# Performance work log

Hardware: AMD Instinct MI355X
Metric: run time of the kernel (lower is better)

The kernel has to match this reference:

```python
import jax, jax.numpy as jnp
import numpy as np

NUM_HEADS = 16
NUM_KV_HEADS = 8
HEAD_DIM = 128
ROPE_THETA = 10000.0
SOFTCAP = 50.0


def rotate_half(x):
    x1, x2 = jnp.split(x, 2, axis=-1)
    return jnp.concatenate((-x2, x1), axis=-1)


def rope_cos_sin(seq_len):
    inv_freq = 1.0 / (ROPE_THETA ** (jnp.arange(0, HEAD_DIM, 2, dtype=jnp.float32) / HEAD_DIM))
    t = jnp.arange(seq_len, dtype=jnp.float32)
    freqs = t[:, None] * inv_freq[None, :]          # [S, D/2]
    emb = jnp.concatenate((freqs, freqs), axis=-1)  # [S, D]
    return jnp.cos(emb), jnp.sin(emb)


def setup_inputs() -> dict:
    key = jax.random.key(0)
    k1, k2, k3, k4, k5 = jax.random.split(key, 5)
    B, S, H = 2, 2048, 2048
    sc = 1.0 / np.sqrt(H)
    return {
        "hidden_states": jax.random.normal(k1, (B, S, H), dtype=jnp.float32),
        "Wq": jax.random.normal(k2, (H, NUM_HEADS * HEAD_DIM), dtype=jnp.float32) * sc,
        "Wk": jax.random.normal(k3, (H, NUM_KV_HEADS * HEAD_DIM), dtype=jnp.float32) * sc,
        "Wv": jax.random.normal(k4, (H, NUM_KV_HEADS * HEAD_DIM), dtype=jnp.float32) * sc,
        "Wo": jax.random.normal(k5, (NUM_HEADS * HEAD_DIM, H), dtype=jnp.float32) * sc,
    }


def reference(hidden_states, Wq, Wk, Wv, Wo):
    B, S, _ = hidden_states.shape
    groups = NUM_HEADS // NUM_KV_HEADS

    # projections -> [B, heads, S, D]
    q = (hidden_states @ Wq).reshape(B, S, NUM_HEADS, HEAD_DIM).transpose(0, 2, 1, 3)
    k = (hidden_states @ Wk).reshape(B, S, NUM_KV_HEADS, HEAD_DIM).transpose(0, 2, 1, 3)
    v = (hidden_states @ Wv).reshape(B, S, NUM_KV_HEADS, HEAD_DIM).transpose(0, 2, 1, 3)

    cos, sin = rope_cos_sin(S)  # [S, D], broadcast over (B, heads)
    q = q * cos + rotate_half(q) * sin
    k = k * cos + rotate_half(k) * sin

    # GQA: expand KV heads (repeat_interleave along head dim)
    k = jnp.repeat(k, groups, axis=1)
    v = jnp.repeat(v, groups, axis=1)

    scores = jnp.einsum('bhsd,bhtd->bhst', q, k) / np.sqrt(HEAD_DIM)
    scores = jnp.tanh(scores / SOFTCAP) * SOFTCAP  # Gemma logit softcapping
    weights = jax.nn.softmax(scores.astype(jnp.float32), axis=-1).astype(q.dtype)

    out = jnp.einsum('bhst,bhtd->bhsd', weights, v)
    out = out.transpose(0, 2, 1, 3).reshape(B, S, NUM_HEADS * HEAD_DIM)
    return out @ Wo
```

## Files before the change

kernel.cpp:

```cpp
#include <hip/hip_runtime.h>
#include <math.h>

typedef __bf16 bf16;
typedef __bf16 bf16x8 __attribute__((ext_vector_type(8)));
typedef __bf16 bf16x4 __attribute__((ext_vector_type(4)));
typedef float f32x2 __attribute__((ext_vector_type(2)));
typedef float f32x4 __attribute__((ext_vector_type(4)));
typedef float f32x16 __attribute__((ext_vector_type(16)));
typedef unsigned int uint;
typedef uint u32x4 __attribute__((ext_vector_type(4)));
typedef uint u32x2 __attribute__((ext_vector_type(2)));
typedef __bf16 bf16x8_a __attribute__((ext_vector_type(8), __may_alias__));
typedef uint u32x2_a __attribute__((ext_vector_type(2), __may_alias__));
typedef __bf16 bf16_a __attribute__((__may_alias__));

constexpr int BATCH = 2;
constexpr int SEQ   = 2048;
constexpr int HID   = 2048;
constexpr int NHEAD = 16;
constexpr int NKV   = 8;
constexpr int HD    = 128;
constexpr int MROWS = BATCH * SEQ;

#define DEVINL __device__ __forceinline__

#define BAR()                                 \
  do {                                        \
    asm volatile("" ::: "memory");            \
    __builtin_amdgcn_s_barrier();             \
    asm volatile("" ::: "memory");            \
  } while (0)

#define WAITV(N) asm volatile("s_waitcnt vmcnt(" #N ")" ::: "memory")

DEVINL void async16(void* l, const void* g) {
  __builtin_amdgcn_global_load_lds((const __attribute__((address_space(1))) void*)g,
                                   (__attribute__((address_space(3))) void*)l, 16, 0, 0);
}

DEVINL f32x4 mfma16(bf16x8 a, bf16x8 b, f32x4 c) {
  return __builtin_amdgcn_mfma_f32_16x16x32_bf16(a, b, c, 0, 0, 0);
}
DEVINL f32x16 mfma32(bf16x8 a, bf16x8 b, f32x16 c) {
  return __builtin_amdgcn_mfma_f32_32x32x16_bf16(a, b, c, 0, 0, 0);
}

DEVINL f32x4 fzero4() { f32x4 z; z[0] = 0.f; z[1] = 0.f; z[2] = 0.f; z[3] = 0.f; return z; }

DEVINL float ex2(float x) {
#if __has_builtin(__builtin_amdgcn_exp2f)
  return __builtin_amdgcn_exp2f(x);
#else
  return __expf(x * 0.6931471805599453f);
#endif
}

DEVINL uint pkbf16(float lo, float hi) {
  unsigned short l = __builtin_bit_cast(unsigned short, (bf16)lo);
  unsigned short h = __builtin_bit_cast(unsigned short, (bf16)hi);
  return (uint)l | ((uint)h << 16);
}

__global__ __launch_bounds__(256) void cast_f32_bf16(const float* __restrict__ x,
                                                     bf16* __restrict__ y, int n) {
  int i = (blockIdx.x * 256 + threadIdx.x) * 4;
  if (i + 3 < n) {
    float4 v = *(const float4*)(x + i);
    bf16x4 o;
    o[0] = (bf16)v.x; o[1] = (bf16)v.y; o[2] = (bf16)v.z; o[3] = (bf16)v.w;
    *(bf16x4*)(y + i) = o;
  }
}

__global__ __launch_bounds__(256) void wtrans4(const float* __restrict__ Wq,
                                               const float* __restrict__ Wk,
                                               const float* __restrict__ Wv,
                                               const float* __restrict__ Wo,
                                               bf16* __restrict__ WqT, bf16* __restrict__ WkT,
                                               bf16* __restrict__ WvT, bf16* __restrict__ WoT) {
  __shared__ bf16 t[64][65];
  const float* W; bf16* WT; int N;
  switch (blockIdx.z) {
    case 0: W = Wq; WT = WqT; N = 2048; break;
    case 1: W = Wk; WT = WkT; N = 1024; break;
    case 2: W = Wv; WT = WvT; N = 1024; break;
    default: W = Wo; WT = WoT; N = 2048; break;
  }
  int n0 = blockIdx.x * 64, k0 = blockIdx.y * 64;
  if (n0 >= N) return;
  for (int i = threadIdx.x; i < 4096; i += 256) {
    int r = i >> 6, c = i & 63;
    t[r][c] = (bf16)W[(size_t)(k0 + r) * N + n0 + c];
  }
  __syncthreads();
  for (int i = threadIdx.x; i < 4096; i += 256) {
    int r = i >> 6, c = i & 63;
    WT[(size_t)(n0 + r) * 2048 + k0 + c] = t[c][r];
  }
}

__global__ __launch_bounds__(256) void vtrans(const bf16* __restrict__ V, bf16* __restrict__ VT) {
  __shared__ bf16 t[64][65];
  int s0 = blockIdx.x * 64, d0 = blockIdx.y * 64;
  int bh = blockIdx.z, b = bh >> 3, kvh = bh & 7;
  for (int i = threadIdx.x; i < 4096; i += 256) {
    int r = i >> 6, c = i & 63;
    t[r][c] = V[(size_t)(b * SEQ + s0 + r) * (NKV * HD) + kvh * HD + d0 + c];
  }
  __syncthreads();
  for (int i = threadIdx.x; i < 4096; i += 256) {
    int r = i >> 6, c = i & 63;
    VT[((size_t)bh * HD + d0 + r) * SEQ + s0 + c] = t[c][r];
  }
}

__global__ void rope_tab(float* __restrict__ ct, float* __restrict__ st) {
  int s = blockIdx.x, d = threadIdx.x;
  float freq = powf(10000.0f, -(float)d * (1.0f / 64.0f));
  float a = (float)s * freq;
  ct[s * 64 + d] = cosf(a);
  st[s * 64 + d] = sinf(a);
}

template <int EPI>
__global__ __launch_bounds__(512, 2) void gemm8p(const bf16* __restrict__ A,
                                                 const bf16* __restrict__ BT,
                                                 void* __restrict__ C0, void* __restrict__ C1,
                                                 void* __restrict__ C2, int M, int N, int K,
                                                 const float* __restrict__ ct,
                                                 const float* __restrict__ st) {
  __shared__ alignas(16) char ldsA[65536];
  __shared__ alignas(16) char ldsB[65536];
  const int tid = threadIdx.x, lane = tid & 63, w = tid >> 6;
  const int l15 = lane & 15, l4 = lane >> 4;
  const int wm = w >> 2, wn = w & 3;
  const int gx = gridDim.x;
  const int nwg = gx * gridDim.y;
  int id = blockIdx.y * gx + blockIdx.x;
  id = (id & 7) * (nwg >> 3) + (id >> 3);
  const int row0 = (id / gx) * 256;
  const int col0 = (id % gx) * 256;

  f32x4 acc[8][4];
#pragma unroll
  for (int mt = 0; mt < 8; mt++)
#pragma unroll
    for (int nt = 0; nt < 4; nt++) acc[mt][nt] = fzero4();

  const int rG0 = tid >> 3, sG0 = ((tid & 7) ^ (rG0 & 7)) * 8;
  const int ci1 = 512 + tid;
  const int rG1 = ci1 >> 3, sG1 = ((ci1 & 7) ^ (rG1 & 7)) * 8;
  const int dst0 = tid * 16, dst1 = (512 + tid) * 16;

  const bf16* Asrc = A + (size_t)row0 * K;
  const bf16* Bsrc = BT + (size_t)col0 * K;
  const int nk = K >> 6;

#define STG_A(half, kt, buf)                                         \
  {                                                                  \
    char* d = ldsA + (buf) * 32768 + (half) * 16384;                 \
    const bf16* s = Asrc + (size_t)((half) * 128) * K + (kt) * 64;   \
    async16(d + dst0, s + (size_t)rG0 * K + sG0);                    \
    async16(d + dst1, s + (size_t)rG1 * K + sG1);                    \
  }
#define STG_B(half, kt, buf)                                         \
  {                                                                  \
    char* d = ldsB + (buf) * 32768 + (half) * 16384;                 \
    const bf16* s = Bsrc + (size_t)((half) * 128) * K + (kt) * 64;   \
    async16(d + dst0, s + (size_t)rG0 * K + sG0);                    \
    async16(d + dst1, s + (size_t)rG1 * K + sG1);                    \
  }

  STG_A(0, 0, 0) STG_A(1, 0, 0) STG_B(0, 0, 0) STG_B(1, 0, 0)
  STG_B(0, 1, 1) STG_B(1, 1, 1) STG_A(0, 1, 1) STG_A(1, 1, 1)
  WAITV(8);
  BAR();

  bf16x8 af[8];
  bf16x8 bfr[2][4];

  for (int t = 0; t < nk; ++t) {
    const int buf = t & 1;
    const char* bA = ldsA + buf * 32768 + wm * 16384;
    const char* bB = ldsB + buf * 32768;
    const bool s2 = (t + 2) < nk;

#pragma unroll
    for (int mtp = 0; mtp < 4; mtp++)
#pragma unroll
      for (int kc = 0; kc < 2; kc++) {
        int r = mtp * 16 + l15;
        int off = ((r << 7) + ((kc * 4 + l4) << 4)) ^ ((r & 7) << 4);
        af[mtp * 2 + kc] = *(const bf16x8_a*)(bA + off);
      }
#pragma unroll
    for (int ntp = 0; ntp < 2; ntp++)
#pragma unroll
      for (int kc = 0; kc < 2; kc++) {
        int c = wn * 16 + ntp * 64 + l15;
        int off = ((c << 7) + ((kc * 4 + l4) << 4)) ^ ((c & 7) << 4);
        bfr[0][ntp * 2 + kc] = *(const bf16x8_a*)(bB + off);
      }
    BAR();
    __builtin_amdgcn_s_setprio(1);
#pragma unroll
    for (int mtp = 0; mtp < 4; mtp++)
#pragma unroll
      for (int ntp = 0; ntp < 2; ntp++)
#pragma unroll
        for (int kc = 0; kc < 2; kc++)
          acc[mtp][ntp] = mfma16(af[mtp * 2 + kc], bfr[0][ntp * 2 + kc], acc[mtp][ntp]);
    __builtin_amdgcn_s_setprio(0);
    BAR();

#pragma unroll
    for (int ntp = 0; ntp < 2; ntp++)
#pragma unroll
      for (int kc = 0; kc < 2; kc++) {
        int c = wn * 16 + ntp * 64 + l15;
        int off = 16384 + (((c << 7) + ((kc * 4 + l4) << 4)) ^ ((c & 7) << 4));
        bfr[1][ntp * 2 + kc] = *(const bf16x8_a*)(bB + off);
      }
    if (s2) STG_B(0, t + 2, buf)
    BAR();
    __builtin_amdgcn_s_setprio(1);
#pragma unroll
    for (int mtp = 0; mtp < 4; mtp++)
#pragma unroll
      for (int ntp = 0; ntp < 2; ntp++)
#pragma unroll
        for (int kc = 0; kc < 2; kc++)
          acc[mtp][ntp + 2] = mfma16(af[mtp * 2 + kc], bfr[1][ntp * 2 + kc], acc[mtp][ntp + 2]);
    __builtin_amdgcn_s_setprio(0);
    BAR();

#pragma unroll
    for (int mtp = 0; mtp < 4; mtp++)
#pragma unroll
      for (int kc = 0; kc < 2; kc++) {
        int r = 64 + mtp * 16 + l15;
        int off = ((r << 7) + ((kc * 4 + l4) << 4)) ^ ((r & 7) << 4);
        af[mtp * 2 + kc] = *(const bf16x8_a*)(bA + off);
      }
    if (s2) STG_B(1, t + 2, buf)
    BAR();
    __builtin_amdgcn_s_setprio(1);
#pragma unroll
    for (int mtp = 0; mtp < 4; mtp++)
#pragma unroll
      for (int ntp = 0; ntp < 2; ntp++)
#pragma unroll
        for (int kc = 0; kc < 2; kc++)
          acc[mtp + 4][ntp + 2] = mfma16(af[mtp * 2 + kc], bfr[1][ntp * 2 + kc], acc[mtp + 4][ntp + 2]);
    __builtin_amdgcn_s_setprio(0);
    BAR();

    if (s2) { STG_A(0, t + 2, buf) STG_A(1, t + 2, buf) }
    BAR();
    __builtin_amdgcn_s_setprio(1);
#pragma unroll
    for (int mtp = 0; mtp < 4; mtp++)
#pragma unroll
      for (int ntp = 0; ntp < 2; ntp++)
#pragma unroll
        for (int kc = 0; kc < 2; kc++)
          acc[mtp + 4][ntp] = mfma16(af[mtp * 2 + kc], bfr[0][ntp * 2 + kc], acc[mtp + 4][ntp]);
    __builtin_amdgcn_s_setprio(0);
    if (s2) { WAITV(8); } else { WAITV(0); }
    BAR();
  }
#undef STG_A
#undef STG_B

#pragma unroll
  for (int mt = 0; mt < 8; mt++)
#pragma unroll
    for (int nt = 0; nt < 4; nt++)
#pragma unroll
      for (int rg = 0; rg < 4; rg++) {
        int row = row0 + wm * 128 + mt * 16 + l4 * 4 + rg;
        int cl = col0 + wn * 16 + nt * 64 + l15;
        float v = acc[mt][nt][rg];
        if (EPI == 2) {
          ((float*)C0)[(size_t)row * N + cl] = v;
        } else {
          if (cl < 3072) {
            int s = row & (SEQ - 1);
            float cc = ct[s * 64 + wn * 16 + l15];
            float ss = st[s * 64 + wn * 16 + l15];
            float pv = acc[mt][nt ^ 1][rg];
            v = (nt & 1) ? fmaf(v, cc, pv * ss) : fmaf(v, cc, -pv * ss);
          }
          if (cl < 2048)
            ((bf16*)C0)[(size_t)row * 2048 + cl] = (bf16)v;
          else if (cl < 3072)
            ((bf16*)C1)[(size_t)row * 1024 + (cl - 2048)] = (bf16)v;
          else
            ((bf16*)C2)[(size_t)row * 1024 + (cl - 3072)] = (bf16)v;
        }
      }
}

__global__ __launch_bounds__(512, 2) void gemm2p(const bf16* __restrict__ A,
                                                 const bf16* __restrict__ BT,
                                                 float* __restrict__ C, int M, int N, int K) {
  __shared__ alignas(16) char ldsA[65536];
  __shared__ alignas(16) char ldsB[32768];
  const int tid = threadIdx.x, lane = tid & 63, w = tid >> 6;
  const int l15 = lane & 15, l4 = lane >> 4;
  const int wm = w >> 1, wn = w & 1;
  const int gx = gridDim.x;
  const int nwg = gx * gridDim.y;
  int id = blockIdx.y * gx + blockIdx.x;
  id = (id & 7) * (nwg >> 3) + (id >> 3);
  const int row0 = (id / gx) * 256;
  const int col0 = (id % gx) * 128;

  f32x4 acc[4][4];
#pragma unroll
  for (int mt = 0; mt < 4; mt++)
#pragma unroll
    for (int nt = 0; nt < 4; nt++) acc[mt][nt] = fzero4();

  const int rG0 = tid >> 3, sG0 = ((tid & 7) ^ (rG0 & 7)) * 8;
  const int ci1 = 512 + tid;
  const int rG1 = ci1 >> 3, sG1 = ((ci1 & 7) ^ (rG1 & 7)) * 8;
  const int dst0 = tid * 16, dst1 = (512 + tid) * 16;

  const bf16* Asrc = A + (size_t)row0 * K;
  const bf16* Bsrc = BT + (size_t)col0 * K;
  const int nk = K >> 6;

#define STG_A2(half, kt, buf)                                        \
  {                                                                  \
    char* d = ldsA + (buf) * 32768 + (half) * 16384;                 \
    const bf16* s = Asrc + (size_t)((half) * 128) * K + (kt) * 64;   \
    async16(d + dst0, s + (size_t)rG0 * K + sG0);                    \
    async16(d + dst1, s + (size_t)rG1 * K + sG1);                    \
  }
#define STG_B2(kt, buf)                                              \
  {                                                                  \
    char* d = ldsB + (buf) * 16384;                                  \
    const bf16* s = Bsrc + (kt) * 64;                                \
    async16(d + dst0, s + (size_t)rG0 * K + sG0);                    \
    async16(d + dst1, s + (size_t)rG1 * K + sG1);                    \
  }

  STG_A2(0, 0, 0) STG_A2(1, 0, 0) STG_B2(0, 0)
  STG_A2(0, 1, 1) STG_A2(1, 1, 1)
  WAITV(4);
  BAR();

  bf16x8 af[8];
  bf16x8 bfr[8];

  for (int t = 0; t < nk; ++t) {
    const int buf = t & 1;
    const char* bA = ldsA + buf * 32768 + (wm >> 1) * 16384;
    const char* bB = ldsB + buf * 16384;
    const bool s1 = (t + 1) < nk;
    const bool s2 = (t + 2) < nk;

#pragma unroll
    for (int mt = 0; mt < 4; mt++)
#pragma unroll
      for (int kc = 0; kc < 2; kc++) {
        int r = (wm & 1) * 64 + mt * 16 + l15;
        int off = ((r << 7) + ((kc * 4 + l4) << 4)) ^ ((r & 7) << 4);
        af[mt * 2 + kc] = *(const bf16x8_a*)(bA + off);
      }
#pragma unroll
    for (int nt = 0; nt < 2; nt++)
#pragma unroll
      for (int kc = 0; kc < 2; kc++) {
        int c = wn * 16 + nt * 32 + l15;
        int off = ((c << 7) + ((kc * 4 + l4) << 4)) ^ ((c & 7) << 4);
        bfr[nt * 2 + kc] = *(const bf16x8_a*)(bB + off);
      }
    if (s1) STG_B2(t + 1, buf ^ 1)
    BAR();
    __builtin_amdgcn_s_setprio(1);
#pragma unroll
    for (int mt = 0; mt < 4; mt++)
#pragma unroll
      for (int nt = 0; nt < 2; nt++)
#pragma unroll
        for (int kc = 0; kc < 2; kc++)
          acc[mt][nt] = mfma16(af[mt * 2 + kc], bfr[nt * 2 + kc], acc[mt][nt]);
    __builtin_amdgcn_s_setprio(0);
    BAR();

#pragma unroll
    for (int nt = 0; nt < 2; nt++)
#pragma unroll
      for (int kc = 0; kc < 2; kc++) {
        int c = wn * 16 + (nt + 2) * 32 + l15;
        int off = ((c << 7) + ((kc * 4 + l4) << 4)) ^ ((c & 7) << 4);
        bfr[4 + nt * 2 + kc] = *(const bf16x8_a*)(bB + off);
      }
    if (s2) { STG_A2(0, t + 2, buf) STG_A2(1, t + 2, buf) }
    BAR();
    __builtin_amdgcn_s_setprio(1);
#pragma unroll
    for (int mt = 0; mt < 4; mt++)
#pragma unroll
      for (int nt = 0; nt < 2; nt++)
#pragma unroll
        for (int kc = 0; kc < 2; kc++)
          acc[mt][nt + 2] = mfma16(af[mt * 2 + kc], bfr[4 + nt * 2 + kc], acc[mt][nt + 2]);
    __builtin_amdgcn_s_setprio(0);
    if (s2) { WAITV(4); } else { WAITV(0); }
    BAR();
  }
#undef STG_A2
#undef STG_B2

#pragma unroll
  for (int mt = 0; mt < 4; mt++)
#pragma unroll
    for (int nt = 0; nt < 4; nt++)
#pragma unroll
      for (int rg = 0; rg < 4; rg++) {
        int row = row0 + wm * 64 + mt * 16 + l4 * 4 + rg;
        int cl = col0 + wn * 16 + nt * 32 + l15;
        C[(size_t)row * N + cl] = acc[mt][nt][rg];
      }
}

__global__ __launch_bounds__(256, 2) void attn5(const bf16* __restrict__ Q,
                                                const bf16* __restrict__ Kg,
                                                const bf16* __restrict__ VTg,
                                                bf16* __restrict__ O) {
  __shared__ alignas(16) char ldsK[32768];
  __shared__ alignas(16) char ldsV[32768];
  const int tid = threadIdx.x, lane = tid & 63, w = tid >> 6;
  const int l31 = lane & 31, hl = lane >> 5;

  const int nx = gridDim.x, ny = gridDim.y;
  const int nwg = nx * ny * gridDim.z;
  int id = (blockIdx.z * ny + blockIdx.y) * nx + blockIdx.x;
  id = (id & 7) * (nwg >> 3) + (id >> 3);
  const int qt = id % nx; id /= nx;
  const int h = id % ny; const int b = id / ny;
  const int kvh = h >> 1;
  const int qrow = b * SEQ + qt * 128 + w * 32 + l31;

  bf16x8 qf[8];
  const bf16* qp = Q + (size_t)qrow * (NHEAD * HD) + h * HD + hl * 8;
#pragma unroll
  for (int kc = 0; kc < 8; kc++) qf[kc] = *(const bf16x8_a*)(qp + kc * 16);

  f32x16 oT[4];
#pragma unroll
  for (int dt = 0; dt < 4; dt++)
#pragma unroll
    for (int r = 0; r < 16; r++) oT[dt][r] = 0.f;
  f32x2 ls2; ls2[0] = 0.f; ls2[1] = 0.f;

  const int dstc = tid * 16;
  const int rK = tid >> 4, lsK = (tid & 15) ^ rK;
  const int rV = tid >> 3, lsV = (tid & 7) ^ (rV & 7);
  const size_t koff0 = (size_t)(b * SEQ + rK) * (NKV * HD) + kvh * HD + lsK * 8;
  const size_t voff0 = ((size_t)(b * NKV + kvh) * HD + rV) * SEQ + lsV * 8;

  const float C1 = 1.7677669529663689e-3f;
  const float CA = -0.33333333333f;
  const float CB = 0.13333333333f;
  const float C2 = 72.13475204444817f;

  auto STAGE = [&](int buf, int t) {
    char* dK = ldsK + buf * 16384 + dstc;
    char* dV = ldsV + buf * 16384 + dstc;
    const bf16* ks = Kg + koff0 + (size_t)t * (64 * NKV * HD);
    const bf16* vs = VTg + voff0 + (size_t)t * 64;
#pragma unroll
    for (int j = 0; j < 4; j++) async16(dK + j * 4096, ks + j * 16 * (NKV * HD));
#pragma unroll
    for (int j = 0; j < 4; j++) async16(dV + j * 4096, vs + (size_t)j * 32 * SEQ);
  };

  STAGE(0, 0);
  WAITV(0);
  BAR();

  for (int t = 0; t < SEQ / 64; ++t) {
    const int cur = t & 1;
    STAGE(cur ^ 1, (t + 1) & (SEQ / 64 - 1));

    const char* lK = ldsK + cur * 16384;
    const char* lV = ldsV + cur * 16384;

    f32x16 sc[2];
#pragma unroll
    for (int r = 0; r < 16; r++) { sc[0][r] = 0.f; sc[1][r] = 0.f; }
    const int kvr0 = l31;
    const int kvr1 = 32 + l31;
    __builtin_amdgcn_s_setprio(1);
#pragma unroll
    for (int kc = 0; kc < 8; kc++) {
      int slot = kc * 2 + hl;
      int off0 = (kvr0 << 8) | ((slot ^ (kvr0 & 15)) << 4);
      int off1 = (kvr1 << 8) | ((slot ^ (kvr1 & 15)) << 4);
      bf16x8 kf0 = *(const bf16x8_a*)(lK + off0);
      bf16x8 kf1 = *(const bf16x8_a*)(lK + off1);
      sc[0] = mfma32(kf0, qf[kc], sc[0]);
      sc[1] = mfma32(kf1, qf[kc], sc[1]);
    }
    __builtin_amdgcn_s_setprio(0);

#pragma unroll
    for (int ntb = 0; ntb < 2; ntb++) {
      uint u[4][2], us[4][2];
#pragma unroll
      for (int r2 = 0; r2 < 8; r2++) {
        f32x2 s2; s2[0] = sc[ntb][2 * r2]; s2[1] = sc[ntb][2 * r2 + 1];
        f32x2 z = s2 * C1;
        f32x2 z2 = z * z;
        f32x2 wv = z2 * (z2 * CB + CA) + 1.0f;
        f32x2 e = (z * wv) * C2;
        float p0 = ex2(e[0]), p1 = ex2(e[1]);
        ls2[0] += p0; ls2[1] += p1;
        uint uu = pkbf16(p0, p1);
        u[r2 >> 1][r2 & 1] = uu;
        us[r2 >> 1][r2 & 1] = __shfl_xor(uu, 32);
      }
      __builtin_amdgcn_s_setprio(1);
#pragma unroll
      for (int sub = 0; sub < 2; sub++) {
        u32x4 bu;
        bu[0] = hl ? us[2 * sub + 1][0] : u[2 * sub][0];
        bu[1] = hl ? us[2 * sub + 1][1] : u[2 * sub][1];
        bu[2] = hl ? u[2 * sub + 1][0] : us[2 * sub][0];
        bu[3] = hl ? u[2 * sub + 1][1] : us[2 * sub][1];
        bf16x8 pb = __builtin_bit_cast(bf16x8, bu);
        const int kvb = ntb * 2 + sub;
        const int slot = kvb * 2 + hl;
#pragma unroll
        for (int dt = 0; dt < 4; dt++) {
          int d = dt * 32 + l31;
          int off = (d << 7) | ((slot ^ (d & 7)) << 4);
          bf16x8 vf = *(const bf16x8_a*)(lV + off);
          oT[dt] = mfma32(vf, pb, oT[dt]);
        }
      }
      __builtin_amdgcn_s_setprio(0);
    }

    WAITV(0);
    BAR();
  }

  float lsum = ls2[0] + ls2[1];
  float lsf = lsum + __shfl_xor(lsum, 32);
  float inv = 1.0f / lsf;
  bf16* ob = O + (size_t)qrow * (NHEAD * HD) + h * HD;
#pragma unroll
  for (int dt = 0; dt < 4; dt++)
#pragma unroll
    for (int g = 0; g < 4; g++) {
      u32x2 pr;
      pr[0] = pkbf16(oT[dt][4 * g] * inv, oT[dt][4 * g + 1] * inv);
      pr[1] = pkbf16(oT[dt][4 * g + 2] * inv, oT[dt][4 * g + 3] * inv);
      *(u32x2_a*)(ob + dt * 32 + 8 * g + 4 * hl) = pr;
    }
}

extern "C" void kernel_launch(void* const* d_in, const int* in_sizes, int n_in,
                              void* d_out, int out_size, void* d_ws, size_t ws_size,
                              hipStream_t stream) {
  const float* X  = (const float*)d_in[0];
  const float* Wq = (const float*)d_in[1];
  const float* Wk = (const float*)d_in[2];
  const float* Wv = (const float*)d_in[3];
  const float* Wo = (const float*)d_in[4];
  float* out = (float*)d_out;

  char* ws = (char*)d_ws;
  size_t off = 0;
  auto alloc = [&](size_t bytes) {
    void* p = ws + off;
    off += (bytes + 255) & ~(size_t)255;
    return p;
  };
  bf16* Xb  = (bf16*)alloc((size_t)MROWS * HID * 2);
  bf16* WqT = (bf16*)alloc((size_t)2048 * 2048 * 2);
  bf16* WkT = (bf16*)alloc((size_t)1024 * 2048 * 2);
  bf16* WvT = (bf16*)alloc((size_t)1024 * 2048 * 2);
  bf16* WoT = (bf16*)alloc((size_t)2048 * 2048 * 2);
  bf16* Qb  = (bf16*)alloc((size_t)MROWS * 2048 * 2);
  bf16* Kb  = (bf16*)alloc((size_t)MROWS * 1024 * 2);
  bf16* Vb  = (bf16*)alloc((size_t)MROWS * 1024 * 2);
  bf16* VTb = (bf16*)alloc((size_t)16 * 128 * 2048 * 2);
  bf16* AOb = (bf16*)alloc((size_t)MROWS * 2048 * 2);
  float* ct = (float*)alloc((size_t)SEQ * 64 * 4);
  float* st = (float*)alloc((size_t)SEQ * 64 * 4);

  cast_f32_bf16<<<(MROWS * HID) / 1024, 256, 0, stream>>>(X, Xb, MROWS * HID);
  wtrans4<<<dim3(32, 32, 4), 256, 0, stream>>>(Wq, Wk, Wv, Wo, WqT, WkT, WvT, WoT);
  rope_tab<<<SEQ, 64, 0, stream>>>(ct, st);
  gemm8p<1><<<dim3(16, 16), 512, 0, stream>>>(Xb, WqT, Qb, Kb, Vb, MROWS, 4096, 2048, ct, st);
  vtrans<<<dim3(32, 2, 16), 256, 0, stream>>>(Vb, VTb);
  attn5<<<dim3(16, 16, 2), 256, 0, stream>>>(Qb, Kb, VTb, AOb);
  gemm2p<<<dim3(16, 16), 512, 0, stream>>>(AOb, WoT, out, MROWS, 2048, 2048);

  (void)in_sizes; (void)n_in; (void)out_size; (void)ws_size;
}
```

Before: 258.0 us.

## Restructure attention to 16x16 MFMA with 8 waves and LDS-staged probabilities

```diff
diff --git a/kernel.cpp b/kernel.cpp
--- a/kernel.cpp
+++ b/kernel.cpp
@@ -40,9 +40,6 @@
 
 DEVINL f32x4 mfma16(bf16x8 a, bf16x8 b, f32x4 c) {
   return __builtin_amdgcn_mfma_f32_16x16x32_bf16(a, b, c, 0, 0, 0);
-}
-DEVINL f32x16 mfma32(bf16x8 a, bf16x8 b, f32x16 c) {
-  return __builtin_amdgcn_mfma_f32_32x32x16_bf16(a, b, c, 0, 0, 0);
 }
 
 DEVINL f32x4 fzero4() { f32x4 z; z[0] = 0.f; z[1] = 0.f; z[2] = 0.f; z[3] = 0.f; return z; }
@@ -291,12 +288,14 @@
             float pv = acc[mt][nt ^ 1][rg];
             v = (nt & 1) ? fmaf(v, cc, pv * ss) : fmaf(v, cc, -pv * ss);
           }
-          if (cl < 2048)
+          if (cl < 2048) {
+            v *= 1.7677669529663689e-3f;
             ((bf16*)C0)[(size_t)row * 2048 + cl] = (bf16)v;
-          else if (cl < 3072)
+          } else if (cl < 3072) {
             ((bf16*)C1)[(size_t)row * 1024 + (cl - 2048)] = (bf16)v;
-          else
+          } else {
             ((bf16*)C2)[(size_t)row * 1024 + (cl - 3072)] = (bf16)v;
+          }
         }
       }
 }
@@ -427,14 +426,15 @@
       }
 }
 
-__global__ __launch_bounds__(256, 2) void attn5(const bf16* __restrict__ Q,
+__global__ __launch_bounds__(512, 4) void attn6(const bf16* __restrict__ Q,
                                                 const bf16* __restrict__ Kg,
                                                 const bf16* __restrict__ VTg,
                                                 bf16* __restrict__ O) {
   __shared__ alignas(16) char ldsK[32768];
   __shared__ alignas(16) char ldsV[32768];
+  __shared__ alignas(16) char ldsP[16384];
   const int tid = threadIdx.x, lane = tid & 63, w = tid >> 6;
-  const int l31 = lane & 31, hl = lane >> 5;
+  const int l15 = lane & 15, l4 = lane >> 4;
 
   const int nx = gridDim.x, ny = gridDim.y;
   const int nwg = nx * ny * gridDim.z;
@@ -443,40 +443,37 @@
   const int qt = id % nx; id /= nx;
   const int h = id % ny; const int b = id / ny;
   const int kvh = h >> 1;
-  const int qrow = b * SEQ + qt * 128 + w * 32 + l31;
-
-  bf16x8 qf[8];
-  const bf16* qp = Q + (size_t)qrow * (NHEAD * HD) + h * HD + hl * 8;
-#pragma unroll
-  for (int kc = 0; kc < 8; kc++) qf[kc] = *(const bf16x8_a*)(qp + kc * 16);
-
-  f32x16 oT[4];
-#pragma unroll
-  for (int dt = 0; dt < 4; dt++)
-#pragma unroll
-    for (int r = 0; r < 16; r++) oT[dt][r] = 0.f;
-  f32x2 ls2; ls2[0] = 0.f; ls2[1] = 0.f;
-
-  const int dstc = tid * 16;
-  const int rK = tid >> 4, lsK = (tid & 15) ^ rK;
-  const int rV = tid >> 3, lsV = (tid & 7) ^ (rV & 7);
-  const size_t koff0 = (size_t)(b * SEQ + rK) * (NKV * HD) + kvh * HD + lsK * 8;
-  const size_t voff0 = ((size_t)(b * NKV + kvh) * HD + rV) * SEQ + lsV * 8;
-
-  const float C1 = 1.7677669529663689e-3f;
-  const float CA = -0.33333333333f;
-  const float CB = 0.13333333333f;
-  const float C2 = 72.13475204444817f;
+  const int qrow = b * SEQ + qt * 128 + w * 16 + l15;
+
+  bf16x8 qf[4];
+  const bf16* qp = Q + (size_t)qrow * (NHEAD * HD) + h * HD + l4 * 8;
+#pragma unroll
+  for (int kc = 0; kc < 4; kc++) qf[kc] = *(const bf16x8_a*)(qp + kc * 32);
+
+  f32x4 oT[8];
+#pragma unroll
+  for (int dt = 0; dt < 8; dt++) oT[dt] = fzero4();
+  f32x4 ls4 = fzero4();
+
+  const int rK = tid >> 4, sK = (tid & 15) ^ (rK & 15);
+  const int rV = tid >> 3, sV = (tid & 7) ^ (rV & 7);
+  const size_t koff0 = (size_t)(b * SEQ + rK) * (NKV * HD) + kvh * HD + sK * 8;
+  const size_t voff0 = ((size_t)(b * NKV + kvh) * HD + rV) * SEQ + sV * 8;
+
+  char* myP = ldsP + w * 2048;
+  const float Ac = 72.13475204444817f;
+  const float Bc = -24.044917348149389f;
+  const float Cc = 9.6179669392597558f;
 
   auto STAGE = [&](int buf, int t) {
-    char* dK = ldsK + buf * 16384 + dstc;
-    char* dV = ldsV + buf * 16384 + dstc;
+    char* dK = ldsK + buf * 16384;
+    char* dV = ldsV + buf * 16384;
     const bf16* ks = Kg + koff0 + (size_t)t * (64 * NKV * HD);
     const bf16* vs = VTg + voff0 + (size_t)t * 64;
-#pragma unroll
-    for (int j = 0; j < 4; j++) async16(dK + j * 4096, ks + j * 16 * (NKV * HD));
-#pragma unroll
-    for (int j = 0; j < 4; j++) async16(dV + j * 4096, vs + (size_t)j * 32 * SEQ);
+    async16(dK + tid * 16, ks);
+    async16(dK + (512 + tid) * 16, ks + (size_t)32 * (NKV * HD));
+    async16(dV + tid * 16, vs);
+    async16(dV + (512 + tid) * 16, vs + (size_t)64 * SEQ);
   };
 
   STAGE(0, 0);
@@ -490,79 +487,81 @@
     const char* lK = ldsK + cur * 16384;
     const char* lV = ldsV + cur * 16384;
 
-    f32x16 sc[2];
-#pragma unroll
-    for (int r = 0; r < 16; r++) { sc[0][r] = 0.f; sc[1][r] = 0.f; }
-    const int kvr0 = l31;
-    const int kvr1 = 32 + l31;
-    __builtin_amdgcn_s_setprio(1);
-#pragma unroll
-    for (int kc = 0; kc < 8; kc++) {
-      int slot = kc * 2 + hl;
-      int off0 = (kvr0 << 8) | ((slot ^ (kvr0 & 15)) << 4);
-      int off1 = (kvr1 << 8) | ((slot ^ (kvr1 & 15)) << 4);
-      bf16x8 kf0 = *(const bf16x8_a*)(lK + off0);
-      bf16x8 kf1 = *(const bf16x8_a*)(lK + off1);
-      sc[0] = mfma32(kf0, qf[kc], sc[0]);
-      sc[1] = mfma32(kf1, qf[kc], sc[1]);
+    f32x4 sc[4];
+#pragma unroll
+    for (int rt = 0; rt < 4; rt++) sc[rt] = fzero4();
+    __builtin_amdgcn_s_setprio(1);
+#pragma unroll
+    for (int rt = 0; rt < 4; rt++) {
+#pragma unroll
+      for (int kc = 0; kc < 4; kc++) {
+        int r = rt * 16 + l15;
+        int slot = kc * 4 + l4;
+        int off = (r << 8) | ((slot ^ (r & 15)) << 4);
+        bf16x8 kf = *(const bf16x8_a*)(lK + off);
+        sc[rt] = mfma16(kf, qf[kc], sc[rt]);
+      }
     }
     __builtin_amdgcn_s_setprio(0);
 
 #pragma unroll
-    for (int ntb = 0; ntb < 2; ntb++) {
-      uint u[4][2], us[4][2];
-#pragma unroll
-      for (int r2 = 0; r2 < 8; r2++) {
-        f32x2 s2; s2[0] = sc[ntb][2 * r2]; s2[1] = sc[ntb][2 * r2 + 1];
-        f32x2 z = s2 * C1;
-        f32x2 z2 = z * z;
-        f32x2 wv = z2 * (z2 * CB + CA) + 1.0f;
-        f32x2 e = (z * wv) * C2;
-        float p0 = ex2(e[0]), p1 = ex2(e[1]);
-        ls2[0] += p0; ls2[1] += p1;
-        uint uu = pkbf16(p0, p1);
-        u[r2 >> 1][r2 & 1] = uu;
-        us[r2 >> 1][r2 & 1] = __shfl_xor(uu, 32);
-      }
-      __builtin_amdgcn_s_setprio(1);
-#pragma unroll
-      for (int sub = 0; sub < 2; sub++) {
-        u32x4 bu;
-        bu[0] = hl ? us[2 * sub + 1][0] : u[2 * sub][0];
-        bu[1] = hl ? us[2 * sub + 1][1] : u[2 * sub][1];
-        bu[2] = hl ? u[2 * sub + 1][0] : us[2 * sub][0];
-        bu[3] = hl ? u[2 * sub + 1][1] : us[2 * sub][1];
-        bf16x8 pb = __builtin_bit_cast(bf16x8, bu);
-        const int kvb = ntb * 2 + sub;
-        const int slot = kvb * 2 + hl;
-#pragma unroll
-        for (int dt = 0; dt < 4; dt++) {
-          int d = dt * 32 + l31;
-          int off = (d << 7) | ((slot ^ (d & 7)) << 4);
-          bf16x8 vf = *(const bf16x8_a*)(lV + off);
-          oT[dt] = mfma32(vf, pb, oT[dt]);
-        }
-      }
-      __builtin_amdgcn_s_setprio(0);
+    for (int rt = 0; rt < 4; rt++) {
+      f32x4 z = sc[rt];
+      f32x4 z2 = z * z;
+      f32x4 wv = z2 * (z2 * Cc + Bc) + Ac;
+      f32x4 e = z * wv;
+      f32x4 p;
+      p[0] = ex2(e[0]); p[1] = ex2(e[1]); p[2] = ex2(e[2]); p[3] = ex2(e[3]);
+      ls4 += p;
+      u32x2 pw;
+      pw[0] = pkbf16(p[0], p[1]);
+      pw[1] = pkbf16(p[2], p[3]);
+      int slot = 2 * rt + (l4 >> 1);
+      int off = (l15 << 7) | ((slot ^ (l15 & 7)) << 4) | ((l4 & 1) << 3);
+      *(u32x2_a*)(myP + off) = pw;
     }
+    asm volatile("s_waitcnt lgkmcnt(0)" ::: "memory");
+    __builtin_amdgcn_sched_barrier(0);
+
+    bf16x8 pf[2];
+#pragma unroll
+    for (int kc = 0; kc < 2; kc++) {
+      int slot = kc * 4 + l4;
+      int off = (l15 << 7) | ((slot ^ (l15 & 7)) << 4);
+      pf[kc] = *(const bf16x8_a*)(myP + off);
+    }
+
+    __builtin_amdgcn_s_setprio(1);
+#pragma unroll
+    for (int dt = 0; dt < 8; dt++) {
+#pragma unroll
+      for (int kc = 0; kc < 2; kc++) {
+        int d = dt * 16 + l15;
+        int slot = kc * 4 + l4;
+        int off = (d << 7) | ((slot ^ (d & 7)) << 4);
+        bf16x8 vf = *(const bf16x8_a*)(lV + off);
+        oT[dt] = mfma16(vf, pf[kc], oT[dt]);
+      }
+    }
+    __builtin_amdgcn_s_setprio(0);
 
     WAITV(0);
     BAR();
   }
 
-  float lsum = ls2[0] + ls2[1];
-  float lsf = lsum + __shfl_xor(lsum, 32);
-  float inv = 1.0f / lsf;
-  bf16* ob = O + (size_t)qrow * (NHEAD * HD) + h * HD;
-#pragma unroll
-  for (int dt = 0; dt < 4; dt++)
-#pragma unroll
-    for (int g = 0; g < 4; g++) {
-      u32x2 pr;
-      pr[0] = pkbf16(oT[dt][4 * g] * inv, oT[dt][4 * g + 1] * inv);
-      pr[1] = pkbf16(oT[dt][4 * g + 2] * inv, oT[dt][4 * g + 3] * inv);
-      *(u32x2_a*)(ob + dt * 32 + 8 * g + 4 * hl) = pr;
-    }
+  float lsum = ls4[0] + ls4[1] + ls4[2] + ls4[3];
+  lsum += __shfl_xor(lsum, 16);
+  lsum += __shfl_xor(lsum, 32);
+  float inv = 1.0f / lsum;
+
+  bf16* ob = O + (size_t)qrow * (NHEAD * HD) + h * HD + l4 * 4;
+#pragma unroll
+  for (int dt = 0; dt < 8; dt++) {
+    u32x2 pr;
+    pr[0] = pkbf16(oT[dt][0] * inv, oT[dt][1] * inv);
+    pr[1] = pkbf16(oT[dt][2] * inv, oT[dt][3] * inv);
+    *(u32x2_a*)(ob + dt * 16) = pr;
+  }
 }
 
 extern "C" void kernel_launch(void* const* d_in, const int* in_sizes, int n_in,
@@ -600,7 +599,7 @@
   rope_tab<<<SEQ, 64, 0, stream>>>(ct, st);
   gemm8p<1><<<dim3(16, 16), 512, 0, stream>>>(Xb, WqT, Qb, Kb, Vb, MROWS, 4096, 2048, ct, st);
   vtrans<<<dim3(32, 2, 16), 256, 0, stream>>>(Vb, VTb);
-  attn5<<<dim3(16, 16, 2), 256, 0, stream>>>(Qb, Kb, VTb, AOb);
+  attn6<<<dim3(16, 16, 2), 512, 0, stream>>>(Qb, Kb, VTb, AOb);
   gemm2p<<<dim3(16, 16), 512, 0, stream>>>(AOb, WoT, out, MROWS, 2048, 2048);
 
   (void)in_sizes; (void)n_in; (void)out_size; (void)ws_size;
```

Result: faster. 251.4 us (-2.5%).

## Widen attention blocks to 256 queries with triple-buffered KV staging

Applied to the files above, without the earlier changes.

```diff
diff --git a/kernel.cpp b/kernel.cpp
--- a/kernel.cpp
+++ b/kernel.cpp
@@ -291,12 +291,14 @@
             float pv = acc[mt][nt ^ 1][rg];
             v = (nt & 1) ? fmaf(v, cc, pv * ss) : fmaf(v, cc, -pv * ss);
           }
-          if (cl < 2048)
+          if (cl < 2048) {
+            v *= 1.7677669529663689e-3f;
             ((bf16*)C0)[(size_t)row * 2048 + cl] = (bf16)v;
-          else if (cl < 3072)
+          } else if (cl < 3072) {
             ((bf16*)C1)[(size_t)row * 1024 + (cl - 2048)] = (bf16)v;
-          else
+          } else {
             ((bf16*)C2)[(size_t)row * 1024 + (cl - 3072)] = (bf16)v;
+          }
         }
       }
 }
@@ -427,12 +429,12 @@
       }
 }
 
-__global__ __launch_bounds__(256, 2) void attn5(const bf16* __restrict__ Q,
+__global__ __launch_bounds__(512, 2) void attn7(const bf16* __restrict__ Q,
                                                 const bf16* __restrict__ Kg,
                                                 const bf16* __restrict__ VTg,
                                                 bf16* __restrict__ O) {
-  __shared__ alignas(16) char ldsK[32768];
-  __shared__ alignas(16) char ldsV[32768];
+  __shared__ alignas(16) char ldsK[49152];
+  __shared__ alignas(16) char ldsV[49152];
   const int tid = threadIdx.x, lane = tid & 63, w = tid >> 6;
   const int l31 = lane & 31, hl = lane >> 5;
 
@@ -443,7 +445,7 @@
   const int qt = id % nx; id /= nx;
   const int h = id % ny; const int b = id / ny;
   const int kvh = h >> 1;
-  const int qrow = b * SEQ + qt * 128 + w * 32 + l31;
+  const int qrow = b * SEQ + qt * 256 + w * 32 + l31;
 
   bf16x8 qf[8];
   const bf16* qp = Q + (size_t)qrow * (NHEAD * HD) + h * HD + hl * 8;
@@ -457,35 +459,38 @@
     for (int r = 0; r < 16; r++) oT[dt][r] = 0.f;
   f32x2 ls2; ls2[0] = 0.f; ls2[1] = 0.f;
 
-  const int dstc = tid * 16;
-  const int rK = tid >> 4, lsK = (tid & 15) ^ rK;
-  const int rV = tid >> 3, lsV = (tid & 7) ^ (rV & 7);
-  const size_t koff0 = (size_t)(b * SEQ + rK) * (NKV * HD) + kvh * HD + lsK * 8;
-  const size_t voff0 = ((size_t)(b * NKV + kvh) * HD + rV) * SEQ + lsV * 8;
-
-  const float C1 = 1.7677669529663689e-3f;
-  const float CA = -0.33333333333f;
-  const float CB = 0.13333333333f;
-  const float C2 = 72.13475204444817f;
+  const int rK = tid >> 4, sK = (tid & 15) ^ (rK & 15);
+  const int rV = tid >> 3, sV = (tid & 7) ^ (rV & 7);
+  const size_t koff0 = (size_t)(b * SEQ + rK) * (NKV * HD) + kvh * HD + sK * 8;
+  const size_t voff0 = ((size_t)(b * NKV + kvh) * HD + rV) * SEQ + sV * 8;
+
+  const float Ac = 72.13475204444817f;
+  const float Bc = -24.044917348149389f;
+  const float Cc = 9.6179669392597558f;
 
   auto STAGE = [&](int buf, int t) {
-    char* dK = ldsK + buf * 16384 + dstc;
-    char* dV = ldsV + buf * 16384 + dstc;
+    char* dK = ldsK + buf * 16384;
+    char* dV = ldsV + buf * 16384;
     const bf16* ks = Kg + koff0 + (size_t)t * (64 * NKV * HD);
     const bf16* vs = VTg + voff0 + (size_t)t * 64;
-#pragma unroll
-    for (int j = 0; j < 4; j++) async16(dK + j * 4096, ks + j * 16 * (NKV * HD));
-#pragma unroll
-    for (int j = 0; j < 4; j++) async16(dV + j * 4096, vs + (size_t)j * 32 * SEQ);
+    async16(dK + tid * 16, ks);
+    async16(dK + (512 + tid) * 16, ks + (size_t)32 * (NKV * HD));
+    async16(dV + tid * 16, vs);
+    async16(dV + (512 + tid) * 16, vs + (size_t)64 * SEQ);
   };
 
+  constexpr int NT = SEQ / 64;
   STAGE(0, 0);
-  WAITV(0);
-  BAR();
-
-  for (int t = 0; t < SEQ / 64; ++t) {
-    const int cur = t & 1;
-    STAGE(cur ^ 1, (t + 1) & (SEQ / 64 - 1));
+  STAGE(1, 1);
+
+  int cur = 0;
+  for (int t = 0; t < NT; ++t) {
+    if (t < NT - 1) { WAITV(8); } else { WAITV(0); }
+    BAR();
+    if (t + 2 < NT) {
+      int nb = cur + 2; if (nb >= 3) nb -= 3;
+      STAGE(nb, t + 2);
+    }
 
     const char* lK = ldsK + cur * 16384;
     const char* lV = ldsV + cur * 16384;
@@ -513,11 +518,10 @@
       uint u[4][2], us[4][2];
 #pragma unroll
       for (int r2 = 0; r2 < 8; r2++) {
-        f32x2 s2; s2[0] = sc[ntb][2 * r2]; s2[1] = sc[ntb][2 * r2 + 1];
-        f32x2 z = s2 * C1;
+        f32x2 z; z[0] = sc[ntb][2 * r2]; z[1] = sc[ntb][2 * r2 + 1];
         f32x2 z2 = z * z;
-        f32x2 wv = z2 * (z2 * CB + CA) + 1.0f;
-        f32x2 e = (z * wv) * C2;
+        f32x2 wv = z2 * (z2 * Cc + Bc) + Ac;
+        f32x2 e = z * wv;
         float p0 = ex2(e[0]), p1 = ex2(e[1]);
         ls2[0] += p0; ls2[1] += p1;
         uint uu = pkbf16(p0, p1);
@@ -546,8 +550,7 @@
       __builtin_amdgcn_s_setprio(0);
     }
 
-    WAITV(0);
-    BAR();
+    cur = (cur == 2) ? 0 : cur + 1;
   }
 
   float lsum = ls2[0] + ls2[1];
@@ -600,7 +603,7 @@
   rope_tab<<<SEQ, 64, 0, stream>>>(ct, st);
   gemm8p<1><<<dim3(16, 16), 512, 0, stream>>>(Xb, WqT, Qb, Kb, Vb, MROWS, 4096, 2048, ct, st);
   vtrans<<<dim3(32, 2, 16), 256, 0, stream>>>(Vb, VTb);
-  attn5<<<dim3(16, 16, 2), 256, 0, stream>>>(Qb, Kb, VTb, AOb);
+  attn7<<<dim3(8, 16, 2), 512, 0, stream>>>(Qb, Kb, VTb, AOb);
   gemm2p<<<dim3(16, 16), 512, 0, stream>>>(AOb, WoT, out, MROWS, 2048, 2048);
 
   (void)in_sizes; (void)n_in; (void)out_size; (void)ws_size;
```

Measured after the change: 251.3 us. -2.6%, faster.
